# Kernel optimization log

Hardware: AMD Instinct MI355X
Metric: run time of the kernel (lower is better)

Reference implementation:

```python
import jax, jax.numpy as jnp
import numpy as np

B, S, D_MODEL = 1, 2048, 2048
H, KVH = 16, 4
HD = D_MODEL // H          # 128
N_REP = H // KVH           # 4 (GQA)
WINDOW = 1024              # window_size=(WINDOW-1, 0): self + 1023 past tokens
CLIP = 8.0
THETA = 500000.0
EPS = 1e-6
SCALE = 1.0 / (HD ** 0.5)


def rms_norm(x, w):
    # per-head RMSNorm over last dim (head_dim)
    var = jnp.mean(jnp.square(x), axis=-1, keepdims=True)
    return x * jax.lax.rsqrt(var + EPS) * w


def rope_tables():
    inv_freq = 1.0 / (THETA ** (jnp.arange(0, HD, 2, dtype=jnp.float32) / HD))
    pos = jnp.arange(S, dtype=jnp.float32)
    freqs = pos[:, None] * inv_freq[None, :]          # [S, HD/2]
    emb = jnp.concatenate([freqs, freqs], axis=-1)    # [S, HD]
    return jnp.cos(emb), jnp.sin(emb)


def rotate_half(x):
    x1, x2 = x[..., : HD // 2], x[..., HD // 2 :]
    return jnp.concatenate([-x2, x1], axis=-1)


def apply_rope(x, cos, sin):
    # x: [B, S, h, HD]; cos/sin: [S, HD]
    return x * cos[None, :, None, :] + rotate_half(x) * sin[None, :, None, :]


def setup_inputs() -> dict:
    key = jax.random.key(0)
    ks = jax.random.split(key, 7)
    w = lambda k, shape: jax.random.normal(k, shape, jnp.float32) * 0.02
    return {
        "x": jax.random.normal(ks[0], (B, S, D_MODEL), jnp.float32),
        "w_q": w(ks[1], (D_MODEL, D_MODEL)),
        "w_k": w(ks[2], (KVH * HD, D_MODEL)),
        "w_v": w(ks[3], (KVH * HD, D_MODEL)),
        "w_out": w(ks[4], (D_MODEL, D_MODEL)),
        "q_norm_w": jnp.ones((HD,), jnp.float32),
        "k_norm_w": jnp.ones((HD,), jnp.float32),
        "sinks": jax.random.normal(ks[5], (H,), jnp.float32),
    }


def reference(x, w_q, w_k, w_v, w_out, q_norm_w, k_norm_w, sinks):
    # fused QKV projection + clip
    q = jnp.clip(x @ w_q.T, -CLIP, CLIP).reshape(B, S, H, HD)
    k = jnp.clip(x @ w_k.T, -CLIP, CLIP).reshape(B, S, KVH, HD)
    v = jnp.clip(x @ w_v.T, -CLIP, CLIP).reshape(B, S, KVH, HD)

    # per-head qk RMSNorm, then RoPE
    q = rms_norm(q, q_norm_w)
    k = rms_norm(k, k_norm_w)
    cos, sin = rope_tables()
    q = apply_rope(q, cos, sin)
    k = apply_rope(k, cos, sin)

    # GQA: repeat_interleave kv heads
    k = jnp.repeat(k, N_REP, axis=2)  # [B, S, H, HD]
    v = jnp.repeat(v, N_REP, axis=2)

    # sliding-window causal attention with a learned per-head sink logit
    logits = jnp.einsum("bqhd,bkhd->bhqk", q, k) * SCALE  # [B, H, S, S]
    qi = jnp.arange(S)[:, None]
    ki = jnp.arange(S)[None, :]
    mask = (ki <= qi) & (ki > qi - WINDOW)                # causal + window
    logits = jnp.where(mask[None, None, :, :], logits, -jnp.inf)

    # sink token: always-visible extra logit sinks[h] with zero value vector
    sink_col = jnp.broadcast_to(sinks[None, :, None, None], (B, H, S, 1))
    full = jnp.concatenate([logits, sink_col], axis=-1)   # [B, H, S, S+1]
    probs = jax.nn.softmax(full, axis=-1)

    att = jnp.einsum("bhqk,bkhd->bqhd", probs[..., :S], v)  # sink value is 0
    return att.reshape(B, S, D_MODEL) @ w_out.T
```

## Files before the change

### kernel.cpp

```cpp
#include <hip/hip_runtime.h>
#include <hip/hip_bf16.h>
#include <math.h>

#define S_LEN 2048
#define DMODEL 2048
#define NH 16
#define NKVH 4
#define HDIM 128
#define WINDOW 1024

typedef __bf16 bf16;
typedef __bf16 bf16x8 __attribute__((ext_vector_type(8)));
typedef float floatx4 __attribute__((ext_vector_type(4)));

static __device__ __forceinline__ bf16x8 load_bf8(const bf16* p) {
    return *reinterpret_cast<const bf16x8*>(p);
}

static __device__ __forceinline__ void async16(const bf16* g, bf16* l) {
    __builtin_amdgcn_global_load_lds(
        (const __attribute__((address_space(1))) void*)g,
        (__attribute__((address_space(3))) void*)l, 16, 0, 0);
}

__global__ __launch_bounds__(256) void convert_kernel(
    const float* __restrict__ x, const float* __restrict__ wq,
    const float* __restrict__ wk, const float* __restrict__ wv,
    const float* __restrict__ wo,
    bf16* __restrict__ xb, bf16* __restrict__ wqb, bf16* __restrict__ wkb,
    bf16* __restrict__ wvb, bf16* __restrict__ wob) {
    int i = blockIdx.x * blockDim.x + threadIdx.x;
    const float* src; bf16* dst; int off;
    if      (i < 1048576) { src = x;  dst = xb;  off = i; }
    else if (i < 2097152) { src = wq; dst = wqb; off = i - 1048576; }
    else if (i < 2359296) { src = wk; dst = wkb; off = i - 2097152; }
    else if (i < 2621440) { src = wv; dst = wvb; off = i - 2359296; }
    else if (i < 3670016) { src = wo; dst = wob; off = i - 2621440; }
    else return;
    float4 v = reinterpret_cast<const float4*>(src)[off];
    union { bf16 b[4]; ushort4 u; } t;
    t.b[0] = (bf16)v.x; t.b[1] = (bf16)v.y; t.b[2] = (bf16)v.z; t.b[3] = (bf16)v.w;
    reinterpret_cast<ushort4*>(dst)[off] = t.u;
}

#define GEMM_BODY(EXTRA_LDS_DECLS)                                             \
    __shared__ __align__(16) bf16 smem[4 * 128 * 64];               \
    EXTRA_LDS_DECLS                                                            \
    int tid = threadIdx.x;                                                     \
    int lane = tid & 63, wid = tid >> 6;                                       \
    int l15 = lane & 15, quad = lane >> 4;                                     \
    int rlocal = lane >> 3;                                                    \
    int scol = ((lane & 7) ^ rlocal) * 8;                                      \
    const bf16* gA = A + (size_t)(m0 + wid * 32 + rlocal) * K + scol;          \
    const bf16* gB = B + (size_t)(n0 + wid * 32 + rlocal) * K + scol;          \
    int ldsOf = (wid * 32) * 64;                                               \
    floatx4 acc[4][4];                                                         \
    _Pragma("unroll") for (int mi = 0; mi < 4; ++mi)                           \
        _Pragma("unroll") for (int ni = 0; ni < 4; ++ni)                       \
            acc[mi][ni] = floatx4{0.f, 0.f, 0.f, 0.f};                         \
    int mb = (wid & 1) * 64, nb = (wid >> 1) * 64;                             \
    _Pragma("unroll") for (int j = 0; j < 4; ++j) {                            \
        async16(gA + (size_t)(j * 8) * K, smem + ldsOf + j * 512);             \
        async16(gB + (size_t)(j * 8) * K, smem + 16384 + ldsOf + j * 512);     \
    }                                                                          \
    int buf = 0;                                                               \
    for (int k0 = 0; k0 < K; k0 += 64) {                                       \
        __syncthreads();                                                       \
        if (k0 + 64 < K) {                                                     \
            int nof = (buf ^ 1) * 8192;                                        \
            _Pragma("unroll") for (int j = 0; j < 4; ++j) {                    \
                async16(gA + (size_t)(j * 8) * K + k0 + 64,                    \
                        smem + nof + ldsOf + j * 512);                         \
                async16(gB + (size_t)(j * 8) * K + k0 + 64,                    \
                        smem + 16384 + nof + ldsOf + j * 512);                 \
            }                                                                  \
        }                                                                      \
        const bf16* sA = smem + buf * 8192;                                    \
        const bf16* sB = smem + 16384 + buf * 8192;                            \
        _Pragma("unroll") for (int kc = 0; kc < 2; ++kc) {                     \
            bf16x8 af[4], bq[4];                                               \
            _Pragma("unroll") for (int i = 0; i < 4; ++i) {                    \
                int ch = ((kc << 2) + quad) ^ (l15 & 7);                       \
                af[i] = load_bf8(sA + (mb + i * 16 + l15) * 64 + ch * 8);      \
                bq[i] = load_bf8(sB + (nb + i * 16 + l15) * 64 + ch * 8);      \
            }                                                                  \
            _Pragma("unroll") for (int mi = 0; mi < 4; ++mi)                   \
                _Pragma("unroll") for (int ni = 0; ni < 4; ++ni)               \
                    acc[mi][ni] = __builtin_amdgcn_mfma_f32_16x16x32_bf16(     \
                        af[mi], bq[ni], acc[mi][ni], 0, 0, 0);                 \
        }                                                                      \
        buf ^= 1;                                                              \
    }

__global__ __launch_bounds__(256) void gemm_qkv_fused(
    const bf16* __restrict__ A, const bf16* __restrict__ B,
    const float* __restrict__ qw, const float* __restrict__ kw,
    bf16* __restrict__ qb, bf16* __restrict__ kb, bf16* __restrict__ vtb) {
    const int K = 2048;
    int m0 = blockIdx.y * 128, n0 = blockIdx.x * 128;
    GEMM_BODY(__shared__ float rowss[128][2];)

#pragma unroll
    for (int mi = 0; mi < 4; ++mi)
#pragma unroll
        for (int ni = 0; ni < 4; ++ni)
#pragma unroll
            for (int r = 0; r < 4; ++r)
                acc[mi][ni][r] = fminf(fmaxf(acc[mi][ni][r], -8.0f), 8.0f);

    if (n0 >= 2560) {
#pragma unroll
        for (int mi = 0; mi < 4; ++mi)
#pragma unroll
            for (int ni = 0; ni < 4; ++ni)
#pragma unroll
                for (int r = 0; r < 4; ++r) {
                    int row = m0 + mb + mi * 16 + quad * 4 + r;
                    int n = n0 + nb + ni * 16 + l15;
                    vtb[(size_t)(n - 2560) * 2048 + row] = (bf16)acc[mi][ni][r];
                }
        return;
    }

    __syncthreads();
    bf16 (*xnorm)[128] = (bf16(*)[128])(smem + 16384);

#pragma unroll
    for (int mi = 0; mi < 4; ++mi)
#pragma unroll
        for (int r = 0; r < 4; ++r) {
            float s = 0.f;
#pragma unroll
            for (int ni = 0; ni < 4; ++ni) s += acc[mi][ni][r] * acc[mi][ni][r];
#pragma unroll
            for (int o = 1; o < 16; o <<= 1) s += __shfl_xor(s, o, 64);
            if (l15 == 0) rowss[mb + mi * 16 + quad * 4 + r][wid >> 1] = s;
        }
    __syncthreads();

    const float* nw = (n0 < 2048) ? qw : kw;
#pragma unroll
    for (int mi = 0; mi < 4; ++mi)
#pragma unroll
        for (int r = 0; r < 4; ++r) {
            int row = mb + mi * 16 + quad * 4 + r;
            float var = (rowss[row][0] + rowss[row][1]) * (1.0f / 128.0f);
            float rinv = rsqrtf(var + 1e-6f);
#pragma unroll
            for (int ni = 0; ni < 4; ++ni) {
                int col = nb + ni * 16 + l15;
                float xn = acc[mi][ni][r] * rinv * nw[col];
                acc[mi][ni][r] = xn;
                xnorm[row][col] = (bf16)xn;
            }
        }
    __syncthreads();

    float invf[4];
#pragma unroll
    for (int ni = 0; ni < 4; ++ni) {
        int fi = (nb + ni * 16 + l15) & 63;
        invf[ni] = __expf((float)fi * (-13.122363377404328f / 64.0f));
    }
    bool lowhalf = (nb == 0);
#pragma unroll
    for (int mi = 0; mi < 4; ++mi)
#pragma unroll
        for (int r = 0; r < 4; ++r) {
            int row = mb + mi * 16 + quad * 4 + r;
            float pos = (float)(m0 + row);
#pragma unroll
            for (int ni = 0; ni < 4; ++ni) {
                int col = nb + ni * 16 + l15;
                float ang = pos * invf[ni];
                float c = __cosf(ang), sn = __sinf(ang);
                float part = (float)xnorm[row][col ^ 64];
                float rot = lowhalf ? -part : part;
                float o = acc[mi][ni][r] * c + rot * sn;
                int n = n0 + col;
                int s = m0 + row;
                if (n0 < 2048) qb[(size_t)s * 2048 + n] = (bf16)o;
                else           kb[(size_t)s * 512 + (n - 2048)] = (bf16)o;
            }
        }
}

__global__ __launch_bounds__(256) void gemm_out(
    const bf16* __restrict__ A, const bf16* __restrict__ B,
    float* __restrict__ C) {
    const int K = 2048, N = 2048;
    int m0 = blockIdx.y * 128, n0 = blockIdx.x * 128;
    GEMM_BODY()
#pragma unroll
    for (int mi = 0; mi < 4; ++mi)
#pragma unroll
        for (int ni = 0; ni < 4; ++ni)
#pragma unroll
            for (int r = 0; r < 4; ++r) {
                int m = m0 + mb + mi * 16 + quad * 4 + r;
                int n = n0 + nb + ni * 16 + l15;
                C[(size_t)m * N + n] = acc[mi][ni][r];
            }
}

__global__ __launch_bounds__(256) void attn(
    const bf16* __restrict__ qb, const bf16* __restrict__ kb,
    const bf16* __restrict__ vtb, const float* __restrict__ sinks,
    bf16* __restrict__ attb) {
    __shared__ __align__(16) bf16 sK[2][64 * 128];
    __shared__ __align__(16) bf16 sV[2][128 * 64];
    __shared__ __align__(16) bf16 sP[4][16 * 72];
    int tid = threadIdx.x;
    int lane = tid & 63, wid = tid >> 6;
    int l15 = lane & 15, quad = lane >> 4;
    int h = blockIdx.y, kh = h >> 2;
    int bq0 = blockIdx.x * 64;
    int qw0 = bq0 + wid * 16;
    bf16* myp = sP[wid];

    bf16x8 qf[4];
    const bf16* qrow = qb + (size_t)(qw0 + l15) * 2048 + h * 128 + quad * 8;
#pragma unroll
    for (int kc = 0; kc < 4; ++kc) qf[kc] = load_bf8(qrow + kc * 32);

    floatx4 acc[8];
#pragma unroll
    for (int f = 0; f < 8; ++f) acc[f] = floatx4{0.f, 0.f, 0.f, 0.f};
    float lpart[4] = {0.f, 0.f, 0.f, 0.f};
    int qi_base = qw0 + quad * 4;

    int keyit = wid * 4 + (lane >> 4);
    int gcK = (lane & 15) ^ keyit;
    int dimit = wid * 8 + (lane >> 3);
    int gcV = (lane & 7) ^ ((lane >> 3) & 7);

    int tstart = bq0 - 1024; if (tstart < 0) tstart = 0;
    const bf16* kbase = kb + (size_t)kh * 128;
    const bf16* vbase = vtb + (size_t)kh * 128 * 2048;

#pragma unroll
    for (int r = 0; r < 4; ++r) {
        async16(kbase + (size_t)(tstart + r * 16 + keyit) * 512 + gcK * 8,
                sK[0] + (r * 16 + wid * 4) * 128);
        async16(vbase + (size_t)(r * 32 + dimit) * 2048 + tstart + gcV * 8,
                sV[0] + (r * 32 + wid * 8) * 64);
    }

    int buf = 0;
    for (int t = tstart; t <= bq0; t += 64) {
        __syncthreads();
        if (t + 64 <= bq0) {
#pragma unroll
            for (int r = 0; r < 4; ++r) {
                async16(kbase + (size_t)(t + 64 + r * 16 + keyit) * 512 + gcK * 8,
                        sK[buf ^ 1] + (r * 16 + wid * 4) * 128);
                async16(vbase + (size_t)(r * 32 + dimit) * 2048 + t + 64 + gcV * 8,
                        sV[buf ^ 1] + (r * 32 + wid * 8) * 64);
            }
        }
        bool active = !((t + 63 <= qw0 - WINDOW) || (t > qw0 + 15));
        if (active) {
            floatx4 s[4];
#pragma unroll
            for (int g = 0; g < 4; ++g) s[g] = floatx4{0.f, 0.f, 0.f, 0.f};
#pragma unroll
            for (int g = 0; g < 4; ++g) {
                int key = g * 16 + l15;
#pragma unroll
                for (int kc = 0; kc < 4; ++kc) {
                    int ch = (kc * 4 + quad) ^ l15;
                    bf16x8 b = load_bf8(sK[buf] + key * 128 + ch * 8);
                    s[g] = __builtin_amdgcn_mfma_f32_16x16x32_bf16(qf[kc], b, s[g], 0, 0, 0);
                }
            }
#pragma unroll
            for (int r = 0; r < 4; ++r) {
                int qi = qi_base + r;
                int row = (quad * 4 + r) * 72;
#pragma unroll
                for (int g = 0; g < 4; ++g) {
                    int ki = t + g * 16 + l15;
                    float v = s[g][r] * 0.08838834764831845f;
                    bool ok = (ki <= qi) && (ki > qi - WINDOW);
                    float e = ok ? __expf(v) : 0.0f;
                    lpart[r] += e;
                    myp[row + g * 16 + l15] = (bf16)e;
                }
            }
            bf16x8 pa0 = load_bf8(myp + l15 * 72 + quad * 8);
            bf16x8 pa1 = load_bf8(myp + l15 * 72 + 32 + quad * 8);
#pragma unroll
            for (int f = 0; f < 8; ++f) {
                int dim = f * 16 + l15;
                int ch0 = quad ^ (l15 & 7);
                int ch1 = (4 + quad) ^ (l15 & 7);
                bf16x8 vb0 = load_bf8(sV[buf] + dim * 64 + ch0 * 8);
                bf16x8 vb1 = load_bf8(sV[buf] + dim * 64 + ch1 * 8);
                acc[f] = __builtin_amdgcn_mfma_f32_16x16x32_bf16(pa0, vb0, acc[f], 0, 0, 0);
                acc[f] = __builtin_amdgcn_mfma_f32_16x16x32_bf16(pa1, vb1, acc[f], 0, 0, 0);
            }
        }
        buf ^= 1;
    }

    float sk = __expf(sinks[h]);
#pragma unroll
    for (int r = 0; r < 4; ++r) {
        float rs = lpart[r];
#pragma unroll
        for (int o = 1; o < 16; o <<= 1) rs += __shfl_xor(rs, o, 64);
        float inv = 1.0f / (rs + sk);
        int m = qw0 + quad * 4 + r;
#pragma unroll
        for (int f = 0; f < 8; ++f) {
            attb[(size_t)m * 2048 + h * 128 + f * 16 + l15] = (bf16)(acc[f][r] * inv);
        }
    }
}

extern "C" void kernel_launch(void* const* d_in, const int* in_sizes, int n_in,
                              void* d_out, int out_size, void* d_ws, size_t ws_size,
                              hipStream_t stream) {
    const float* x      = (const float*)d_in[0];
    const float* w_q    = (const float*)d_in[1];
    const float* w_k    = (const float*)d_in[2];
    const float* w_v    = (const float*)d_in[3];
    const float* w_out  = (const float*)d_in[4];
    const float* q_norm = (const float*)d_in[5];
    const float* k_norm = (const float*)d_in[6];
    const float* sinks  = (const float*)d_in[7];

    char* ws = (char*)d_ws;
    const size_t MB = 1u << 20;
    bf16* xb   = (bf16*)(ws + 0 * MB);
    bf16* wqb  = (bf16*)(ws + 8 * MB);
    bf16* wkb  = (bf16*)(ws + 16 * MB);
    bf16* wvb  = (bf16*)(ws + 18 * MB);
    bf16* wob  = (bf16*)(ws + 20 * MB);
    bf16* qb   = (bf16*)(ws + 28 * MB);
    bf16* kb   = (bf16*)(ws + 36 * MB);
    bf16* vtb  = (bf16*)(ws + 38 * MB);
    bf16* attb = (bf16*)(ws + 40 * MB);
    bf16* wcomb = wqb;
    float* out = (float*)d_out;

    convert_kernel<<<14336, 256, 0, stream>>>(x, w_q, w_k, w_v, w_out,
                                              xb, wqb, wkb, wvb, wob);
    gemm_qkv_fused<<<dim3(24, 16), 256, 0, stream>>>(xb, wcomb, q_norm, k_norm,
                                                     qb, kb, vtb);
    attn<<<dim3(32, 16), 256, 0, stream>>>(qb, kb, vtb, sinks, attb);
    gemm_out<<<dim3(16, 16), 256, 0, stream>>>(attb, wob, out);
}
```

Measured before the change: 211.6 us.

## Split attention work by key slice per wave and swap GEMM grid order

The attention kernel now has each wave compute scores for all 64 queries against its own 16-key slice. Probabilities are shared through a block-wide LDS tile so each wave accumulates PV over 32 head dims for all queries, and row sums are reduced across waves at the end. This removes per-wave masking skips and per-wave redundant K/V fragment loads, at the cost of an extra __syncthreads per tile and full work on partially masked tiles. Separately, both GEMM launches swap blockIdx x/y so that consecutive blocks walk along M, which changes L2 reuse of the weight tiles.

```diff
diff --git a/kernel.cpp b/kernel.cpp
--- a/kernel.cpp
+++ b/kernel.cpp
@@ -97,7 +97,7 @@
     const float* __restrict__ qw, const float* __restrict__ kw,
     bf16* __restrict__ qb, bf16* __restrict__ kb, bf16* __restrict__ vtb) {
     const int K = 2048;
-    int m0 = blockIdx.y * 128, n0 = blockIdx.x * 128;
+    int m0 = blockIdx.x * 128, n0 = blockIdx.y * 128;
     GEMM_BODY(__shared__ float rowss[128][2];)
 
 #pragma unroll
@@ -189,7 +189,7 @@
     const bf16* __restrict__ A, const bf16* __restrict__ B,
     float* __restrict__ C) {
     const int K = 2048, N = 2048;
-    int m0 = blockIdx.y * 128, n0 = blockIdx.x * 128;
+    int m0 = blockIdx.x * 128, n0 = blockIdx.y * 128;
     GEMM_BODY()
 #pragma unroll
     for (int mi = 0; mi < 4; ++mi)
@@ -209,25 +209,32 @@
     bf16* __restrict__ attb) {
     __shared__ __align__(16) bf16 sK[2][64 * 128];
     __shared__ __align__(16) bf16 sV[2][128 * 64];
-    __shared__ __align__(16) bf16 sP[4][16 * 72];
+    __shared__ __align__(16) bf16 sP[64 * 72];
+    __shared__ float redu[64][4];
     int tid = threadIdx.x;
     int lane = tid & 63, wid = tid >> 6;
     int l15 = lane & 15, quad = lane >> 4;
     int h = blockIdx.y, kh = h >> 2;
     int bq0 = blockIdx.x * 64;
-    int qw0 = bq0 + wid * 16;
-    bf16* myp = sP[wid];
-
-    bf16x8 qf[4];
-    const bf16* qrow = qb + (size_t)(qw0 + l15) * 2048 + h * 128 + quad * 8;
-#pragma unroll
-    for (int kc = 0; kc < 4; ++kc) qf[kc] = load_bf8(qrow + kc * 32);
-
-    floatx4 acc[8];
-#pragma unroll
-    for (int f = 0; f < 8; ++f) acc[f] = floatx4{0.f, 0.f, 0.f, 0.f};
-    float lpart[4] = {0.f, 0.f, 0.f, 0.f};
-    int qi_base = qw0 + quad * 4;
+
+    bf16x8 qf[4][4];
+#pragma unroll
+    for (int mi = 0; mi < 4; ++mi) {
+        const bf16* qrow = qb + (size_t)(bq0 + mi * 16 + l15) * 2048 + h * 128 + quad * 8;
+#pragma unroll
+        for (int kc = 0; kc < 4; ++kc) qf[mi][kc] = load_bf8(qrow + kc * 32);
+    }
+
+    floatx4 acc[4][2];
+#pragma unroll
+    for (int mi = 0; mi < 4; ++mi)
+#pragma unroll
+        for (int df = 0; df < 2; ++df) acc[mi][df] = floatx4{0.f, 0.f, 0.f, 0.f};
+    float lp[4][4];
+#pragma unroll
+    for (int mi = 0; mi < 4; ++mi)
+#pragma unroll
+        for (int r = 0; r < 4; ++r) lp[mi][r] = 0.f;
 
     int keyit = wid * 4 + (lane >> 4);
     int gcK = (lane & 15) ^ keyit;
@@ -258,64 +265,74 @@
                         sV[buf ^ 1] + (r * 32 + wid * 8) * 64);
             }
         }
-        bool active = !((t + 63 <= qw0 - WINDOW) || (t > qw0 + 15));
-        if (active) {
-            floatx4 s[4];
-#pragma unroll
-            for (int g = 0; g < 4; ++g) s[g] = floatx4{0.f, 0.f, 0.f, 0.f};
-#pragma unroll
-            for (int g = 0; g < 4; ++g) {
-                int key = g * 16 + l15;
-#pragma unroll
-                for (int kc = 0; kc < 4; ++kc) {
-                    int ch = (kc * 4 + quad) ^ l15;
-                    bf16x8 b = load_bf8(sK[buf] + key * 128 + ch * 8);
-                    s[g] = __builtin_amdgcn_mfma_f32_16x16x32_bf16(qf[kc], b, s[g], 0, 0, 0);
-                }
-            }
+        floatx4 S[4];
+#pragma unroll
+        for (int mi = 0; mi < 4; ++mi) S[mi] = floatx4{0.f, 0.f, 0.f, 0.f};
+#pragma unroll
+        for (int kc = 0; kc < 4; ++kc) {
+            int ch = (kc * 4 + quad) ^ l15;
+            bf16x8 kf = load_bf8(sK[buf] + (wid * 16 + l15) * 128 + ch * 8);
+#pragma unroll
+            for (int mi = 0; mi < 4; ++mi)
+                S[mi] = __builtin_amdgcn_mfma_f32_16x16x32_bf16(qf[mi][kc], kf, S[mi], 0, 0, 0);
+        }
+        int ki = t + wid * 16 + l15;
+#pragma unroll
+        for (int mi = 0; mi < 4; ++mi)
 #pragma unroll
             for (int r = 0; r < 4; ++r) {
-                int qi = qi_base + r;
-                int row = (quad * 4 + r) * 72;
-#pragma unroll
-                for (int g = 0; g < 4; ++g) {
-                    int ki = t + g * 16 + l15;
-                    float v = s[g][r] * 0.08838834764831845f;
-                    bool ok = (ki <= qi) && (ki > qi - WINDOW);
-                    float e = ok ? __expf(v) : 0.0f;
-                    lpart[r] += e;
-                    myp[row + g * 16 + l15] = (bf16)e;
-                }
-            }
-            bf16x8 pa0 = load_bf8(myp + l15 * 72 + quad * 8);
-            bf16x8 pa1 = load_bf8(myp + l15 * 72 + 32 + quad * 8);
-#pragma unroll
-            for (int f = 0; f < 8; ++f) {
-                int dim = f * 16 + l15;
-                int ch0 = quad ^ (l15 & 7);
-                int ch1 = (4 + quad) ^ (l15 & 7);
-                bf16x8 vb0 = load_bf8(sV[buf] + dim * 64 + ch0 * 8);
-                bf16x8 vb1 = load_bf8(sV[buf] + dim * 64 + ch1 * 8);
-                acc[f] = __builtin_amdgcn_mfma_f32_16x16x32_bf16(pa0, vb0, acc[f], 0, 0, 0);
-                acc[f] = __builtin_amdgcn_mfma_f32_16x16x32_bf16(pa1, vb1, acc[f], 0, 0, 0);
+                int qi = bq0 + mi * 16 + quad * 4 + r;
+                float v = S[mi][r] * 0.08838834764831845f;
+                bool ok = (ki <= qi) && (ki > qi - WINDOW);
+                float e = ok ? __expf(v) : 0.0f;
+                lp[mi][r] += e;
+                sP[(mi * 16 + quad * 4 + r) * 72 + wid * 16 + l15] = (bf16)e;
+            }
+        __syncthreads();
+#pragma unroll
+        for (int kc = 0; kc < 2; ++kc) {
+            bf16x8 pf[4];
+#pragma unroll
+            for (int mi = 0; mi < 4; ++mi)
+                pf[mi] = load_bf8(sP + (mi * 16 + l15) * 72 + kc * 32 + quad * 8);
+#pragma unroll
+            for (int df = 0; df < 2; ++df) {
+                int dim = wid * 32 + df * 16 + l15;
+                int ch = (kc * 4 + quad) ^ (l15 & 7);
+                bf16x8 vf = load_bf8(sV[buf] + dim * 64 + ch * 8);
+#pragma unroll
+                for (int mi = 0; mi < 4; ++mi)
+                    acc[mi][df] = __builtin_amdgcn_mfma_f32_16x16x32_bf16(pf[mi], vf, acc[mi][df], 0, 0, 0);
             }
         }
         buf ^= 1;
     }
 
+#pragma unroll
+    for (int mi = 0; mi < 4; ++mi)
+#pragma unroll
+        for (int r = 0; r < 4; ++r) {
+            float v = lp[mi][r];
+#pragma unroll
+            for (int o = 1; o < 16; o <<= 1) v += __shfl_xor(v, o, 64);
+            if (l15 == 0) redu[mi * 16 + quad * 4 + r][wid] = v;
+        }
+    __syncthreads();
     float sk = __expf(sinks[h]);
 #pragma unroll
-    for (int r = 0; r < 4; ++r) {
-        float rs = lpart[r];
-#pragma unroll
-        for (int o = 1; o < 16; o <<= 1) rs += __shfl_xor(rs, o, 64);
-        float inv = 1.0f / (rs + sk);
-        int m = qw0 + quad * 4 + r;
-#pragma unroll
-        for (int f = 0; f < 8; ++f) {
-            attb[(size_t)m * 2048 + h * 128 + f * 16 + l15] = (bf16)(acc[f][r] * inv);
-        }
-    }
+    for (int mi = 0; mi < 4; ++mi)
+#pragma unroll
+        for (int r = 0; r < 4; ++r) {
+            int row = mi * 16 + quad * 4 + r;
+            float rs = redu[row][0] + redu[row][1] + redu[row][2] + redu[row][3] + sk;
+            float inv = 1.0f / rs;
+#pragma unroll
+            for (int df = 0; df < 2; ++df) {
+                int dim = wid * 32 + df * 16 + l15;
+                attb[(size_t)(bq0 + row) * 2048 + h * 128 + dim] =
+                    (bf16)(acc[mi][df][r] * inv);
+            }
+        }
 }
 
 extern "C" void kernel_launch(void* const* d_in, const int* in_sizes, int n_in,
@@ -346,7 +363,7 @@
 
     convert_kernel<<<14336, 256, 0, stream>>>(x, w_q, w_k, w_v, w_out,
                                               xb, wqb, wkb, wvb, wob);
-    gemm_qkv_fused<<<dim3(24, 16), 256, 0, stream>>>(xb, wcomb, q_norm, k_norm,
+    gemm_qkv_fused<<<dim3(16, 24), 256, 0, stream>>>(xb, wcomb, q_norm, k_norm,
                                                      qb, kb, vtb);
     attn<<<dim3(32, 16), 256, 0, stream>>>(qb, kb, vtb, sinks, attb);
     gemm_out<<<dim3(16, 16), 256, 0, stream>>>(attb, wob, out);
```

Result: no change. 213.5 us (+0.9%).
